# Kernel tuning notes

Hardware: AMD Instinct MI355X
Metric: run time of the kernel (lower is better)

The kernel has to match this reference:

```python
import jax, jax.numpy as jnp
import numpy as np

N = 50000   # node_count
D = 64      # dim_in (also GCN hidden, GRU hidden, top-k k)
E = 800000  # num_edges


def setup_inputs() -> dict:
    key = jax.random.key(0)
    ks = jax.random.split(key, 10)
    s = 1.0 / np.sqrt(D)
    return {
        "x": jax.random.normal(ks[0], (N, D), jnp.float32),
        "edge_index": jax.random.randint(ks[1], (2, E), 0, N, dtype=jnp.int64),
        "edge_weight": jax.random.uniform(ks[2], (E,), jnp.float32),
        # TopKPooling projection vector p
        "pool_p": jax.random.normal(ks[3], (D,), jnp.float32) * s,
        # EvolveGCNH initial weight (GRU hidden state h0), [D, D]
        "init_W": jax.random.normal(ks[4], (D, D), jnp.float32) * s,
        # GRU params, torch gate order (r, z, n)
        "gru_Wih": jax.random.normal(ks[5], (3 * D, D), jnp.float32) * s,
        "gru_Whh": jax.random.normal(ks[6], (3 * D, D), jnp.float32) * s,
        "gru_bih": jax.random.normal(ks[7], (3 * D,), jnp.float32) * s,
        "gru_bhh": jax.random.normal(ks[8], (3 * D,), jnp.float32) * s,
        # final Linear(D, 1)
        "lin_W": jax.random.normal(ks[9], (1, D), jnp.float32) * s,
        "lin_b": jnp.zeros((1,), jnp.float32),
    }


def reference(x, edge_index, edge_weight, pool_p, init_W,
              gru_Wih, gru_Whh, gru_bih, gru_bhh, lin_W, lin_b):
    n, d = x.shape
    # ---- TopKPooling: k = ceil((D/N) * N) = D nodes ----
    score = (x @ pool_p) / jnp.linalg.norm(pool_p)          # [N]
    vals, perm = jax.lax.top_k(score, d)                    # descending, k = D
    x_tilde = x[perm] * jnp.tanh(vals)[:, None]             # [D, D]
    # ---- one GRU step: batch = D pooled nodes, hidden = D, h0 = init_W ----
    gi = x_tilde @ gru_Wih.T + gru_bih                      # [D, 3D]
    gh = init_W @ gru_Whh.T + gru_bhh                       # [D, 3D]
    i_r, i_z, i_n = jnp.split(gi, 3, axis=-1)
    h_r, h_z, h_n = jnp.split(gh, 3, axis=-1)
    r = jax.nn.sigmoid(i_r + h_r)
    z = jax.nn.sigmoid(i_z + h_z)
    nn_ = jnp.tanh(i_n + r * h_n)
    W = (1.0 - z) * nn_ + z * init_W                        # evolved GCN weight [D, D]
    # ---- GCNConv_Fixed_W: add self-loops + symmetric norm + scatter ----
    loop = jnp.arange(n)
    row = jnp.concatenate([edge_index[0], loop])            # sources
    col = jnp.concatenate([edge_index[1], loop])            # targets
    w = jnp.concatenate([edge_weight, jnp.ones((n,), x.dtype)])
    deg = jax.ops.segment_sum(w, col, num_segments=n)
    deg_safe = jnp.where(deg > 0, deg, 1.0)
    dinv = jnp.where(deg > 0, jax.lax.rsqrt(deg_safe), 0.0)
    norm = dinv[row] * w * dinv[col]                        # [E+N]
    xw = x @ W                                              # [N, D]
    agg = jax.ops.segment_sum(norm[:, None] * xw[row], col, num_segments=n)
    # ---- head: relu + Linear(D, 1) ----
    h = jax.nn.relu(agg)
    return h @ lin_W.T + lin_b                              # [N, 1]
```

## Files before the change

### kernel.cpp

```cpp
#include <hip/hip_runtime.h>
#include <hip/hip_fp16.h>
#include <cmath>

#define N_NODES 50000
#define NPAD 50016
#define DIM 64
#define E_EDGES 800000
#define FIX32 65536.0f
#define NB_A 98
#define NB_EDGE 391
#define ESTRIDE (NB_EDGE * 512)
#define NRUNS 98
#define NXCD 8
#define BUCKET8 24
#define XW_BLOCKS 782

__device__ __forceinline__ int xcc_id() {
    int x;
    asm volatile("s_getreg_b32 %0, hwreg(HW_REG_XCC_ID)" : "=s"(x));
    return x & 7;
}

__device__ __forceinline__ void wave_sort64(float& v, int& idx, int lane) {
    #pragma unroll
    for (int k = 2; k <= 64; k <<= 1) {
        #pragma unroll
        for (int j = k >> 1; j > 0; j >>= 1) {
            float ov = __shfl_xor(v, j);
            int   oi = __shfl_xor(idx, j);
            bool lower = ((lane & j) == 0);
            bool up    = ((lane & k) == 0);
            bool mine_prec = (v > ov) || (v == ov && idx < oi);
            bool keep = up ? (lower == mine_prec) : (lower != mine_prec);
            if (!keep) { v = ov; idx = oi; }
        }
    }
}

__device__ __forceinline__ void wave_merge_top64(float& v, int& idx,
                                                 float bv, int bi, int lane) {
    bool a_prec = (v > bv) || (v == bv && idx < bi);
    if (!a_prec) { v = bv; idx = bi; }
    #pragma unroll
    for (int j = 32; j > 0; j >>= 1) {
        float ov = __shfl_xor(v, j);
        int   oi = __shfl_xor(idx, j);
        bool lower = ((lane & j) == 0);
        bool mine_prec = (v > ov) || (v == ov && idx < oi);
        bool keep = (lower == mine_prec);
        if (!keep) { v = ov; idx = oi; }
    }
}

__global__ __launch_bounds__(512) void score_topk_edge_kernel(
    const float* __restrict__ x, const float* __restrict__ p,
    float* __restrict__ cand_val, int* __restrict__ cand_idx,
    const int* __restrict__ ei, const float* __restrict__ ew,
    unsigned int* __restrict__ packed8, unsigned int* __restrict__ ren8) {
    __shared__ float sv[512];
    __shared__ int   si[512];
    int t = threadIdx.x, lane = t & 63, wvid = t >> 6;
    if (blockIdx.x < NB_A) {
        int g = blockIdx.x * 512 + t;
        float v; int idx;
        if (g < N_NODES) {
            const float4* x4 = (const float4*)(x + (size_t)g * DIM);
            const float4* p4 = (const float4*)p;
            float dot = 0.f, pn = 0.f;
            #pragma unroll
            for (int k = 0; k < 16; k++) {
                float4 xv = x4[k], pv = p4[k];
                dot += xv.x * pv.x + xv.y * pv.y + xv.z * pv.z + xv.w * pv.w;
                pn  += pv.x * pv.x + pv.y * pv.y + pv.z * pv.z + pv.w * pv.w;
            }
            v = dot / sqrtf(pn);
            idx = g;
        } else { v = -INFINITY; idx = 0x7fffffff; }
        wave_sort64(v, idx, lane);
        sv[t] = v; si[t] = idx;
        __syncthreads();
        if (wvid == 0) {
            #pragma unroll
            for (int r = 1; r < 8; r++)
                wave_merge_top64(v, idx, sv[r * 64 + 63 - lane], si[r * 64 + 63 - lane], lane);
            cand_val[blockIdx.x * 64 + lane] = v;
            cand_idx[blockIdx.x * 64 + lane] = idx;
        }
    }
    int xcc = xcc_id();
    unsigned int* mypk  = packed8 + (size_t)xcc * NPAD;
    unsigned int* myren = ren8 + (size_t)xcc * N_NODES * BUCKET8;
    int e0 = blockIdx.x * 512 + t;
    int   rr[4]; int cc[4]; float wwv[4]; bool valid[4];
    #pragma unroll
    for (int k = 0; k < 4; k++) {
        int e = e0 + k * ESTRIDE;
        bool vld = (e < E_EDGES);
        int ie = vld ? e : 0;
        rr[k]  = ei[ie];
        cc[k]  = vld ? ei[E_EDGES + ie] : N_NODES;
        wwv[k] = ew[ie];
        valid[k] = vld;
    }
    unsigned int q[4];
    unsigned int* ap[4];
    #pragma unroll
    for (int k = 0; k < 4; k++) {
        q[k] = valid[k] ? ((1u << 24) | (unsigned int)(wwv[k] * FIX32)) : 0u;
        ap[k] = &mypk[cc[k]];
    }
    unsigned int o0, o1, o2, o3;
    asm volatile(
        "global_atomic_add %0, %4, %8, off sc0\n\t"
        "global_atomic_add %1, %5, %9, off sc0\n\t"
        "global_atomic_add %2, %6, %10, off sc0\n\t"
        "global_atomic_add %3, %7, %11, off sc0\n\t"
        "s_waitcnt vmcnt(0)"
        : "=&v"(o0), "=&v"(o1), "=&v"(o2), "=&v"(o3)
        : "v"(ap[0]), "v"(ap[1]), "v"(ap[2]), "v"(ap[3]),
          "v"(q[0]), "v"(q[1]), "v"(q[2]), "v"(q[3])
        : "memory");
    unsigned int oo[4] = {o0, o1, o2, o3};
    #pragma unroll
    for (int k = 0; k < 4; k++) {
        unsigned int pos = oo[k] >> 24;
        if (valid[k] && pos < BUCKET8) {
            __half hw = __float2half(wwv[k]);
            unsigned int rec = ((unsigned int)__half_as_ushort(hw) << 16) | (unsigned int)rr[k];
            myren[(size_t)cc[k] * BUCKET8 + pos] = rec;
        }
    }
}

__global__ __launch_bounds__(1024) void topk_b_kernel(
    const float* __restrict__ cand_val, const int* __restrict__ cand_idx,
    const float* __restrict__ x, float* __restrict__ x_tilde) {
    __shared__ float rsv[16 * 64];
    __shared__ int   rsi[16 * 64];
    __shared__ float tval[64];
    __shared__ int   perm[64];
    int t = threadIdx.x, lane = t & 63, wv = t >> 6;
    int r0 = wv * 8;
    float v; int idx;
    if (r0 < NRUNS) { v = cand_val[r0 * 64 + lane]; idx = cand_idx[r0 * 64 + lane]; }
    else            { v = -INFINITY; idx = 0x7fffffff; }
    for (int r = r0 + 1; r < r0 + 8 && r < NRUNS; r++)
        wave_merge_top64(v, idx, cand_val[r * 64 + 63 - lane],
                         cand_idx[r * 64 + 63 - lane], lane);
    rsv[wv * 64 + lane] = v; rsi[wv * 64 + lane] = idx;
    __syncthreads();
    if (wv == 0) {
        v = rsv[lane]; idx = rsi[lane];
        for (int r = 1; r < 16; r++)
            wave_merge_top64(v, idx, rsv[r * 64 + 63 - lane],
                             rsi[r * 64 + 63 - lane], lane);
        tval[lane] = tanhf(v);
        perm[lane] = idx;
    }
    __syncthreads();
    for (int i = t; i < 4096; i += 1024) {
        int j = i >> 6, kk = i & 63;
        x_tilde[i] = x[perm[j] * DIM + kk] * tval[j];
    }
}

__global__ __launch_bounds__(256) void gru_kernel(
    const float* __restrict__ xt, const float* __restrict__ initW,
    const float* __restrict__ Wih, const float* __restrict__ Whh,
    const float* __restrict__ bih, const float* __restrict__ bhh,
    float* __restrict__ Wout) {
    __shared__ float xrow_s[256], hrow_s[256];
    int t = threadIdx.x;
    int i = blockIdx.x * 4 + (t >> 6);
    int j = t & 63;
    int li = (t >> 6) * 64 + j;
    xrow_s[li] = xt[i * 64 + j];
    hrow_s[li] = initW[i * 64 + j];
    __syncthreads();
    int lb = (t >> 6) * 64;
    float gi_r = bih[j], gi_z = bih[j + 64], gi_n = bih[j + 128];
    float gh_r = bhh[j], gh_z = bhh[j + 64], gh_n = bhh[j + 128];
    for (int k = 0; k < 64; k++) {
        float xv = xrow_s[lb + k], hv = hrow_s[lb + k];
        gi_r += xv * Wih[j * 64 + k];
        gi_z += xv * Wih[(j + 64) * 64 + k];
        gi_n += xv * Wih[(j + 128) * 64 + k];
        gh_r += hv * Whh[j * 64 + k];
        gh_z += hv * Whh[(j + 64) * 64 + k];
        gh_n += hv * Whh[(j + 128) * 64 + k];
    }
    float r = 1.f / (1.f + expf(-(gi_r + gh_r)));
    float z = 1.f / (1.f + expf(-(gi_z + gh_z)));
    float nn = tanhf(gi_n + r * gh_n);
    Wout[i * 64 + j] = (1.f - z) * nn + z * hrow_s[lb + j];
}

__global__ __launch_bounds__(256) void xw_kernel(
    const float* __restrict__ x, const float* __restrict__ W,
    const unsigned int* __restrict__ packed8, __half* __restrict__ xwh) {
    __shared__ float Wl[64 * 64];
    __shared__ float Xl[64 * 64];
    __shared__ float dinv_s[64];
    int t = threadIdx.x;
    int r0 = blockIdx.x * 64;
    if (t < 64) {
        int r = r0 + t;
        unsigned int s = 0;
        if (r < N_NODES) {
            #pragma unroll
            for (int xx = 0; xx < NXCD; xx++)
                s += packed8[(size_t)xx * NPAD + r] & 0xFFFFFFu;
        }
        dinv_s[t] = rsqrtf((float)s * (1.0f / FIX32) + 1.0f);
    }
    for (int i = t; i < 4096; i += 256) Wl[i] = W[i];
    for (int i = t; i < 4096; i += 256) {
        int r = r0 + (i >> 6);
        Xl[i] = (r < N_NODES) ? x[r0 * 64 + i] : 0.f;
    }
    __syncthreads();
    int j = t & 63, ty = t >> 6;
    float acc[16];
    #pragma unroll
    for (int rr = 0; rr < 16; rr++) acc[rr] = 0.f;
    for (int k = 0; k < 64; k++) {
        float wvv = Wl[k * 64 + j];
        #pragma unroll
        for (int rr = 0; rr < 16; rr++)
            acc[rr] += Xl[(ty * 16 + rr) * 64 + k] * wvv;
    }
    #pragma unroll
    for (int rr = 0; rr < 16; rr++) {
        int r = r0 + ty * 16 + rr;
        if (r < N_NODES)
            xwh[r * DIM + j] = __float2half(acc[rr] * dinv_s[ty * 16 + rr]);
    }
}

__global__ __launch_bounds__(256) void gather_head_kernel(
    const unsigned int* __restrict__ packed8, const unsigned int* __restrict__ ren8,
    const float4* __restrict__ xwh,
    const float* __restrict__ linW, const float* __restrict__ linb,
    float* __restrict__ out) {
    int gid = blockIdx.x * blockDim.x + threadIdx.x;
    int n = gid >> 6, lane = gid & 63;
    if (n >= N_NODES) return;
    int c8 = lane & 7;
    int slot = lane >> 3;
    int xsel = -1, xslot = 0, pref = 0;
    unsigned int wfix = 0;
    #pragma unroll
    for (int xx = 0; xx < NXCD; xx++) {
        unsigned int pkx = packed8[(size_t)xx * NPAD + n];
        int cx = min((int)(pkx >> 24), BUCKET8);
        wfix += pkx & 0xFFFFFFu;
        if (lane >= pref && lane < pref + cx) { xsel = xx; xslot = lane - pref; }
        pref += cx;
    }
    int cnt = min(pref, 64);
    float di = rsqrtf((float)wfix * (1.0f / FIX32) + 1.0f);
    float acc[8];
    #pragma unroll
    for (int q = 0; q < 8; q++) acc[q] = 0.f;
    if (slot == 0) {
        float4 hv = xwh[n * 8 + c8];
        const __half2* h2 = reinterpret_cast<const __half2*>(&hv);
        #pragma unroll
        for (int q = 0; q < 4; q++) {
            float2 f = __half22float2(h2[q]);
            acc[2 * q]     = f.x;
            acc[2 * q + 1] = f.y;
        }
    }
    int rv = 0; float wv = 0.f;
    if (xsel >= 0 && lane < cnt) {
        unsigned int rec = ren8[((size_t)xsel * N_NODES + n) * BUCKET8 + xslot];
        rv = (int)(rec & 0xFFFFu);
        __half_raw hr; hr.x = (unsigned short)(rec >> 16);
        wv = __half2float(__half(hr));
    }
    int G = (cnt + 7) >> 3;
    int g = 0;
    for (; g + 2 <= G; g += 2) {
        int src0 = g * 8 + slot, src1 = src0 + 8;
        int   ra = __shfl(rv, src0);  float wa = __shfl(wv, src0);
        int   rb = __shfl(rv, src1);  float wb = __shfl(wv, src1);
        float4 ha = xwh[ra * 8 + c8];
        float4 hb = xwh[rb * 8 + c8];
        const __half2* h2a = reinterpret_cast<const __half2*>(&ha);
        const __half2* h2b = reinterpret_cast<const __half2*>(&hb);
        #pragma unroll
        for (int q = 0; q < 4; q++) {
            float2 fa = __half22float2(h2a[q]);
            float2 fb = __half22float2(h2b[q]);
            acc[2 * q]     += wa * fa.x + wb * fb.x;
            acc[2 * q + 1] += wa * fa.y + wb * fb.y;
        }
    }
    if (g < G) {
        int src = g * 8 + slot;
        int r = __shfl(rv, src);
        float ww = __shfl(wv, src);
        float4 hv = xwh[r * 8 + c8];
        const __half2* h2 = reinterpret_cast<const __half2*>(&hv);
        #pragma unroll
        for (int q = 0; q < 4; q++) {
            float2 f = __half22float2(h2[q]);
            acc[2 * q]     += ww * f.x;
            acc[2 * q + 1] += ww * f.y;
        }
    }
    #pragma unroll
    for (int q = 0; q < 8; q++) {
        acc[q] += __shfl_xor(acc[q], 8);
        acc[q] += __shfl_xor(acc[q], 16);
        acc[q] += __shfl_xor(acc[q], 32);
    }
    float pv = 0.f;
    #pragma unroll
    for (int q = 0; q < 8; q++)
        pv += fmaxf(di * acc[q], 0.f) * linW[c8 * 8 + q];
    pv += __shfl_xor(pv, 1); pv += __shfl_xor(pv, 2); pv += __shfl_xor(pv, 4);
    if (lane == 0) out[n] = pv + linb[0];
}

extern "C" void kernel_launch(void* const* d_in, const int* in_sizes, int n_in,
                              void* d_out, int out_size, void* d_ws, size_t ws_size,
                              hipStream_t stream) {
    const float* x     = (const float*)d_in[0];
    const int*   ei    = (const int*)d_in[1];
    const float* ew    = (const float*)d_in[2];
    const float* p     = (const float*)d_in[3];
    const float* initW = (const float*)d_in[4];
    const float* Wih   = (const float*)d_in[5];
    const float* Whh   = (const float*)d_in[6];
    const float* bih   = (const float*)d_in[7];
    const float* bhh   = (const float*)d_in[8];
    const float* linW  = (const float*)d_in[9];
    const float* linb  = (const float*)d_in[10];
    float* out = (float*)d_out;

    char* w = (char*)d_ws;
    unsigned int* packed8 = (unsigned int*)w; w += 4ull * NXCD * NPAD;
    unsigned int* ren8 = (unsigned int*)w;    w += 4ull * NXCD * N_NODES * BUCKET8;
    __half* xwh    = (__half*)w;   w += 2ull * (size_t)N_NODES * DIM;
    float* cand_val= (float*)w;    w += 4ull * 8192;
    int*   cand_idx= (int*)w;      w += 4ull * 8192;
    float* x_tilde = (float*)w;    w += 4ull * 4096;
    float* W       = (float*)w;    w += 4ull * 4096;

    hipMemsetAsync(packed8, 0, 4ull * NXCD * NPAD, stream);
    score_topk_edge_kernel<<<NB_EDGE, 512, 0, stream>>>(
        x, p, cand_val, cand_idx, ei, ew, packed8, ren8);
    topk_b_kernel<<<1, 1024, 0, stream>>>(cand_val, cand_idx, x, x_tilde);
    gru_kernel<<<16, 256, 0, stream>>>(x_tilde, initW, Wih, Whh, bih, bhh, W);
    xw_kernel<<<XW_BLOCKS, 256, 0, stream>>>(x, W, packed8, xwh);
    gather_head_kernel<<<(N_NODES * 64 + 255) / 256, 256, 0, stream>>>(
        packed8, ren8, (const float4*)xwh, linW, linb, out);
}
```

Baseline: 205.0 us.

## Fuse top-k merge, GRU, XW and gather into one cooperative persistent kernel

Result: slower. 414.6 us (+102.2%).

```diff
diff --git a/kernel.cpp b/kernel.cpp
--- a/kernel.cpp
+++ b/kernel.cpp
@@ -1,4 +1,5 @@
 #include <hip/hip_runtime.h>
+#include <hip/hip_cooperative_groups.h>
 #include <hip/hip_fp16.h>
 #include <cmath>
 
@@ -14,6 +15,8 @@
 #define NXCD 8
 #define BUCKET8 24
 #define XW_BLOCKS 782
+#define NB_TAIL 512
+
 
 __device__ __forceinline__ int xcc_id() {
     int x;
@@ -132,196 +135,207 @@
     }
 }
 
-__global__ __launch_bounds__(1024) void topk_b_kernel(
+__global__ __launch_bounds__(256) void fused_tail_kernel(
     const float* __restrict__ cand_val, const int* __restrict__ cand_idx,
-    const float* __restrict__ x, float* __restrict__ x_tilde) {
-    __shared__ float rsv[16 * 64];
-    __shared__ int   rsi[16 * 64];
-    __shared__ float tval[64];
-    __shared__ int   perm[64];
+    const float* __restrict__ x, float* __restrict__ x_tilde,
+    const float* __restrict__ initW, const float* __restrict__ Wih,
+    const float* __restrict__ Whh, const float* __restrict__ bih,
+    const float* __restrict__ bhh, float* __restrict__ W,
+    const unsigned int* __restrict__ packed8, const unsigned int* __restrict__ ren8,
+    __half* __restrict__ xwh, const float* __restrict__ linW,
+    const float* __restrict__ linb, float* __restrict__ out) {
+    namespace cg = cooperative_groups;
+    cg::grid_group grid = cg::this_grid();
+    __shared__ float smem[8256];
     int t = threadIdx.x, lane = t & 63, wv = t >> 6;
-    int r0 = wv * 8;
-    float v; int idx;
-    if (r0 < NRUNS) { v = cand_val[r0 * 64 + lane]; idx = cand_idx[r0 * 64 + lane]; }
-    else            { v = -INFINITY; idx = 0x7fffffff; }
-    for (int r = r0 + 1; r < r0 + 8 && r < NRUNS; r++)
-        wave_merge_top64(v, idx, cand_val[r * 64 + 63 - lane],
-                         cand_idx[r * 64 + 63 - lane], lane);
-    rsv[wv * 64 + lane] = v; rsi[wv * 64 + lane] = idx;
-    __syncthreads();
-    if (wv == 0) {
-        v = rsv[lane]; idx = rsi[lane];
-        for (int r = 1; r < 16; r++)
-            wave_merge_top64(v, idx, rsv[r * 64 + 63 - lane],
-                             rsi[r * 64 + 63 - lane], lane);
-        tval[lane] = tanhf(v);
-        perm[lane] = idx;
-    }
-    __syncthreads();
-    for (int i = t; i < 4096; i += 1024) {
-        int j = i >> 6, kk = i & 63;
-        x_tilde[i] = x[perm[j] * DIM + kk] * tval[j];
-    }
-}
-
-__global__ __launch_bounds__(256) void gru_kernel(
-    const float* __restrict__ xt, const float* __restrict__ initW,
-    const float* __restrict__ Wih, const float* __restrict__ Whh,
-    const float* __restrict__ bih, const float* __restrict__ bhh,
-    float* __restrict__ Wout) {
-    __shared__ float xrow_s[256], hrow_s[256];
-    int t = threadIdx.x;
-    int i = blockIdx.x * 4 + (t >> 6);
-    int j = t & 63;
-    int li = (t >> 6) * 64 + j;
-    xrow_s[li] = xt[i * 64 + j];
-    hrow_s[li] = initW[i * 64 + j];
-    __syncthreads();
-    int lb = (t >> 6) * 64;
-    float gi_r = bih[j], gi_z = bih[j + 64], gi_n = bih[j + 128];
-    float gh_r = bhh[j], gh_z = bhh[j + 64], gh_n = bhh[j + 128];
-    for (int k = 0; k < 64; k++) {
-        float xv = xrow_s[lb + k], hv = hrow_s[lb + k];
-        gi_r += xv * Wih[j * 64 + k];
-        gi_z += xv * Wih[(j + 64) * 64 + k];
-        gi_n += xv * Wih[(j + 128) * 64 + k];
-        gh_r += hv * Whh[j * 64 + k];
-        gh_z += hv * Whh[(j + 64) * 64 + k];
-        gh_n += hv * Whh[(j + 128) * 64 + k];
-    }
-    float r = 1.f / (1.f + expf(-(gi_r + gh_r)));
-    float z = 1.f / (1.f + expf(-(gi_z + gh_z)));
-    float nn = tanhf(gi_n + r * gh_n);
-    Wout[i * 64 + j] = (1.f - z) * nn + z * hrow_s[lb + j];
-}
-
-__global__ __launch_bounds__(256) void xw_kernel(
-    const float* __restrict__ x, const float* __restrict__ W,
-    const unsigned int* __restrict__ packed8, __half* __restrict__ xwh) {
-    __shared__ float Wl[64 * 64];
-    __shared__ float Xl[64 * 64];
-    __shared__ float dinv_s[64];
-    int t = threadIdx.x;
-    int r0 = blockIdx.x * 64;
-    if (t < 64) {
-        int r = r0 + t;
-        unsigned int s = 0;
-        if (r < N_NODES) {
-            #pragma unroll
-            for (int xx = 0; xx < NXCD; xx++)
-                s += packed8[(size_t)xx * NPAD + r] & 0xFFFFFFu;
-        }
-        dinv_s[t] = rsqrtf((float)s * (1.0f / FIX32) + 1.0f);
-    }
-    for (int i = t; i < 4096; i += 256) Wl[i] = W[i];
-    for (int i = t; i < 4096; i += 256) {
-        int r = r0 + (i >> 6);
-        Xl[i] = (r < N_NODES) ? x[r0 * 64 + i] : 0.f;
-    }
-    __syncthreads();
-    int j = t & 63, ty = t >> 6;
-    float acc[16];
-    #pragma unroll
-    for (int rr = 0; rr < 16; rr++) acc[rr] = 0.f;
-    for (int k = 0; k < 64; k++) {
-        float wvv = Wl[k * 64 + j];
+    int bx = blockIdx.x;
+
+    if (bx == 0) {
+        float* rsv  = smem;
+        int*   rsi  = (int*)(smem + 256);
+        float* tval = smem + 512;
+        int*   perm = (int*)(smem + 576);
+        float v = cand_val[wv * 64 + lane];
+        int idx   = cand_idx[wv * 64 + lane];
+        for (int r = wv + 4; r < NRUNS; r += 4)
+            wave_merge_top64(v, idx, cand_val[r * 64 + 63 - lane],
+                             cand_idx[r * 64 + 63 - lane], lane);
+        rsv[wv * 64 + lane] = v; rsi[wv * 64 + lane] = idx;
+        __syncthreads();
+        if (wv == 0) {
+            #pragma unroll
+            for (int r = 1; r < 4; r++)
+                wave_merge_top64(v, idx, rsv[r * 64 + 63 - lane],
+                                 rsi[r * 64 + 63 - lane], lane);
+            tval[lane] = tanhf(v);
+            perm[lane] = idx;
+        }
+        __syncthreads();
+        for (int i = t; i < 4096; i += 256) {
+            int j = i >> 6, kk = i & 63;
+            x_tilde[i] = x[(size_t)perm[j] * DIM + kk] * tval[j];
+        }
+    }
+    grid.sync();
+
+    if (bx < 16) {
+        float* xrow_s = smem;
+        float* hrow_s = smem + 256;
+        int i = bx * 4 + wv;
+        int j = lane;
+        int li = wv * 64 + j;
+        xrow_s[li] = x_tilde[i * 64 + j];
+        hrow_s[li] = initW[i * 64 + j];
+        __syncthreads();
+        int lb = wv * 64;
+        float gi_r = bih[j], gi_z = bih[j + 64], gi_n = bih[j + 128];
+        float gh_r = bhh[j], gh_z = bhh[j + 64], gh_n = bhh[j + 128];
+        for (int k = 0; k < 64; k++) {
+            float xv = xrow_s[lb + k], hv = hrow_s[lb + k];
+            gi_r += xv * Wih[j * 64 + k];
+            gi_z += xv * Wih[(j + 64) * 64 + k];
+            gi_n += xv * Wih[(j + 128) * 64 + k];
+            gh_r += hv * Whh[j * 64 + k];
+            gh_z += hv * Whh[(j + 64) * 64 + k];
+            gh_n += hv * Whh[(j + 128) * 64 + k];
+        }
+        float r_ = 1.f / (1.f + expf(-(gi_r + gh_r)));
+        float z_ = 1.f / (1.f + expf(-(gi_z + gh_z)));
+        float nn = tanhf(gi_n + r_ * gh_n);
+        W[i * 64 + j] = (1.f - z_) * nn + z_ * hrow_s[lb + j];
+    }
+    grid.sync();
+
+    {
+        float* Wl     = smem;
+        float* Xl     = smem + 4096;
+        float* dinv_s = smem + 8192;
+        for (int i = t; i < 4096; i += 256) Wl[i] = W[i];
+        for (int tile = bx; tile < XW_BLOCKS; tile += NB_TAIL) {
+            __syncthreads();
+            int r0 = tile * 64;
+            if (t < 64) {
+                int r = r0 + t;
+                unsigned int s = 0;
+                if (r < N_NODES) {
+                    #pragma unroll
+                    for (int xx = 0; xx < NXCD; xx++)
+                        s += packed8[(size_t)xx * NPAD + r] & 0xFFFFFFu;
+                }
+                dinv_s[t] = rsqrtf((float)s * (1.0f / FIX32) + 1.0f);
+            }
+            for (int i = t; i < 4096; i += 256) {
+                int r = r0 + (i >> 6);
+                Xl[i] = (r < N_NODES) ? x[r0 * 64 + i] : 0.f;
+            }
+            __syncthreads();
+            int j = t & 63, ty = t >> 6;
+            float acc[16];
+            #pragma unroll
+            for (int rr = 0; rr < 16; rr++) acc[rr] = 0.f;
+            for (int k = 0; k < 64; k++) {
+                float wvv = Wl[k * 64 + j];
+                #pragma unroll
+                for (int rr = 0; rr < 16; rr++)
+                    acc[rr] += Xl[(ty * 16 + rr) * 64 + k] * wvv;
+            }
+            #pragma unroll
+            for (int rr = 0; rr < 16; rr++) {
+                int r = r0 + ty * 16 + rr;
+                if (r < N_NODES)
+                    xwh[r * DIM + j] = __float2half(acc[rr] * dinv_s[ty * 16 + rr]);
+            }
+        }
+    }
+    grid.sync();
+
+    {
+        const float4* xwh4 = (const float4*)xwh;
+        int gw = bx * 4 + wv;
+        int c8 = lane & 7;
+        int slot = lane >> 3;
+        float lw[8];
         #pragma unroll
-        for (int rr = 0; rr < 16; rr++)
-            acc[rr] += Xl[(ty * 16 + rr) * 64 + k] * wvv;
-    }
-    #pragma unroll
-    for (int rr = 0; rr < 16; rr++) {
-        int r = r0 + ty * 16 + rr;
-        if (r < N_NODES)
-            xwh[r * DIM + j] = __float2half(acc[rr] * dinv_s[ty * 16 + rr]);
-    }
-}
-
-__global__ __launch_bounds__(256) void gather_head_kernel(
-    const unsigned int* __restrict__ packed8, const unsigned int* __restrict__ ren8,
-    const float4* __restrict__ xwh,
-    const float* __restrict__ linW, const float* __restrict__ linb,
-    float* __restrict__ out) {
-    int gid = blockIdx.x * blockDim.x + threadIdx.x;
-    int n = gid >> 6, lane = gid & 63;
-    if (n >= N_NODES) return;
-    int c8 = lane & 7;
-    int slot = lane >> 3;
-    int xsel = -1, xslot = 0, pref = 0;
-    unsigned int wfix = 0;
-    #pragma unroll
-    for (int xx = 0; xx < NXCD; xx++) {
-        unsigned int pkx = packed8[(size_t)xx * NPAD + n];
-        int cx = min((int)(pkx >> 24), BUCKET8);
-        wfix += pkx & 0xFFFFFFu;
-        if (lane >= pref && lane < pref + cx) { xsel = xx; xslot = lane - pref; }
-        pref += cx;
-    }
-    int cnt = min(pref, 64);
-    float di = rsqrtf((float)wfix * (1.0f / FIX32) + 1.0f);
-    float acc[8];
-    #pragma unroll
-    for (int q = 0; q < 8; q++) acc[q] = 0.f;
-    if (slot == 0) {
-        float4 hv = xwh[n * 8 + c8];
-        const __half2* h2 = reinterpret_cast<const __half2*>(&hv);
-        #pragma unroll
-        for (int q = 0; q < 4; q++) {
-            float2 f = __half22float2(h2[q]);
-            acc[2 * q]     = f.x;
-            acc[2 * q + 1] = f.y;
-        }
-    }
-    int rv = 0; float wv = 0.f;
-    if (xsel >= 0 && lane < cnt) {
-        unsigned int rec = ren8[((size_t)xsel * N_NODES + n) * BUCKET8 + xslot];
-        rv = (int)(rec & 0xFFFFu);
-        __half_raw hr; hr.x = (unsigned short)(rec >> 16);
-        wv = __half2float(__half(hr));
-    }
-    int G = (cnt + 7) >> 3;
-    int g = 0;
-    for (; g + 2 <= G; g += 2) {
-        int src0 = g * 8 + slot, src1 = src0 + 8;
-        int   ra = __shfl(rv, src0);  float wa = __shfl(wv, src0);
-        int   rb = __shfl(rv, src1);  float wb = __shfl(wv, src1);
-        float4 ha = xwh[ra * 8 + c8];
-        float4 hb = xwh[rb * 8 + c8];
-        const __half2* h2a = reinterpret_cast<const __half2*>(&ha);
-        const __half2* h2b = reinterpret_cast<const __half2*>(&hb);
-        #pragma unroll
-        for (int q = 0; q < 4; q++) {
-            float2 fa = __half22float2(h2a[q]);
-            float2 fb = __half22float2(h2b[q]);
-            acc[2 * q]     += wa * fa.x + wb * fb.x;
-            acc[2 * q + 1] += wa * fa.y + wb * fb.y;
-        }
-    }
-    if (g < G) {
-        int src = g * 8 + slot;
-        int r = __shfl(rv, src);
-        float ww = __shfl(wv, src);
-        float4 hv = xwh[r * 8 + c8];
-        const __half2* h2 = reinterpret_cast<const __half2*>(&hv);
-        #pragma unroll
-        for (int q = 0; q < 4; q++) {
-            float2 f = __half22float2(h2[q]);
-            acc[2 * q]     += ww * f.x;
-            acc[2 * q + 1] += ww * f.y;
-        }
-    }
-    #pragma unroll
-    for (int q = 0; q < 8; q++) {
-        acc[q] += __shfl_xor(acc[q], 8);
-        acc[q] += __shfl_xor(acc[q], 16);
-        acc[q] += __shfl_xor(acc[q], 32);
-    }
-    float pv = 0.f;
-    #pragma unroll
-    for (int q = 0; q < 8; q++)
-        pv += fmaxf(di * acc[q], 0.f) * linW[c8 * 8 + q];
-    pv += __shfl_xor(pv, 1); pv += __shfl_xor(pv, 2); pv += __shfl_xor(pv, 4);
-    if (lane == 0) out[n] = pv + linb[0];
+        for (int q = 0; q < 8; q++) lw[q] = linW[c8 * 8 + q];
+        float lb0 = linb[0];
+        for (int n = gw; n < N_NODES; n += NB_TAIL * 4) {
+            int xsel = -1, xslot = 0, pref = 0;
+            unsigned int wfix = 0;
+            #pragma unroll
+            for (int xx = 0; xx < NXCD; xx++) {
+                unsigned int pkx = packed8[(size_t)xx * NPAD + n];
+                int cx = min((int)(pkx >> 24), BUCKET8);
+                wfix += pkx & 0xFFFFFFu;
+                if (lane >= pref && lane < pref + cx) { xsel = xx; xslot = lane - pref; }
+                pref += cx;
+            }
+            int cnt = min(pref, 64);
+            float di = rsqrtf((float)wfix * (1.0f / FIX32) + 1.0f);
+            float acc[8];
+            #pragma unroll
+            for (int q = 0; q < 8; q++) acc[q] = 0.f;
+            if (slot == 0) {
+                float4 hv = xwh4[n * 8 + c8];
+                const __half2* h2 = reinterpret_cast<const __half2*>(&hv);
+                #pragma unroll
+                for (int q = 0; q < 4; q++) {
+                    float2 f = __half22float2(h2[q]);
+                    acc[2 * q]     = f.x;
+                    acc[2 * q + 1] = f.y;
+                }
+            }
+            int rv = 0; float wvd = 0.f;
+            if (xsel >= 0 && lane < cnt) {
+                unsigned int rec = ren8[((size_t)xsel * N_NODES + n) * BUCKET8 + xslot];
+                rv = (int)(rec & 0xFFFFu);
+                __half_raw hr; hr.x = (unsigned short)(rec >> 16);
+                wvd = __half2float(__half(hr));
+            }
+            int G = (cnt + 7) >> 3;
+            int g = 0;
+            for (; g + 2 <= G; g += 2) {
+                int src0 = g * 8 + slot, src1 = src0 + 8;
+                int   ra = __shfl(rv, src0);  float wa = __shfl(wvd, src0);
+                int   rb = __shfl(rv, src1);  float wb = __shfl(wvd, src1);
+                float4 ha = xwh4[ra * 8 + c8];
+                float4 hb = xwh4[rb * 8 + c8];
+                const __half2* h2a = reinterpret_cast<const __half2*>(&ha);
+                const __half2* h2b = reinterpret_cast<const __half2*>(&hb);
+                #pragma unroll
+                for (int q = 0; q < 4; q++) {
+                    float2 fa = __half22float2(h2a[q]);
+                    float2 fb = __half22float2(h2b[q]);
+                    acc[2 * q]     += wa * fa.x + wb * fb.x;
+                    acc[2 * q + 1] += wa * fa.y + wb * fb.y;
+                }
+            }
+            if (g < G) {
+                int src = g * 8 + slot;
+                int r = __shfl(rv, src);
+                float ww = __shfl(wvd, src);
+                float4 hv = xwh4[r * 8 + c8];
+                const __half2* h2 = reinterpret_cast<const __half2*>(&hv);
+                #pragma unroll
+                for (int q = 0; q < 4; q++) {
+                    float2 f = __half22float2(h2[q]);
+                    acc[2 * q]     += ww * f.x;
+                    acc[2 * q + 1] += ww * f.y;
+                }
+            }
+            #pragma unroll
+            for (int q = 0; q < 8; q++) {
+                acc[q] += __shfl_xor(acc[q], 8);
+                acc[q] += __shfl_xor(acc[q], 16);
+                acc[q] += __shfl_xor(acc[q], 32);
+            }
+            float pv = 0.f;
+            #pragma unroll
+            for (int q = 0; q < 8; q++)
+                pv += fmaxf(di * acc[q], 0.f) * lw[q];
+            pv += __shfl_xor(pv, 1); pv += __shfl_xor(pv, 2); pv += __shfl_xor(pv, 4);
+            if (lane == 0) out[n] = pv + lb0;
+        }
+    }
 }
 
 extern "C" void kernel_launch(void* const* d_in, const int* in_sizes, int n_in,
@@ -352,9 +366,11 @@
     hipMemsetAsync(packed8, 0, 4ull * NXCD * NPAD, stream);
     score_topk_edge_kernel<<<NB_EDGE, 512, 0, stream>>>(
         x, p, cand_val, cand_idx, ei, ew, packed8, ren8);
-    topk_b_kernel<<<1, 1024, 0, stream>>>(cand_val, cand_idx, x, x_tilde);
-    gru_kernel<<<16, 256, 0, stream>>>(x_tilde, initW, Wih, Whh, bih, bhh, W);
-    xw_kernel<<<XW_BLOCKS, 256, 0, stream>>>(x, W, packed8, xwh);
-    gather_head_kernel<<<(N_NODES * 64 + 255) / 256, 256, 0, stream>>>(
-        packed8, ren8, (const float4*)xwh, linW, linb, out);
-}
+    void* args[] = {
+        (void*)&cand_val, (void*)&cand_idx, (void*)&x, (void*)&x_tilde,
+        (void*)&initW, (void*)&Wih, (void*)&Whh, (void*)&bih, (void*)&bhh,
+        (void*)&W, (void*)&packed8, (void*)&ren8, (void*)&xwh,
+        (void*)&linW, (void*)&linb, (void*)&out };
+    hipLaunchCooperativeKernel((void*)fused_tail_kernel, dim3(NB_TAIL), dim3(256),
+                               args, 0, stream);
+}
```
